# Kernel tuning notes

Hardware: AMD Instinct MI355X
Metric: run time of the kernel (lower is better)

Reference implementation:

```python
import jax, jax.numpy as jnp
import numpy as np

# Model constants (match init_kwargs and fla GatedLinearAttention defaults used in source)
L = 4            # num_layers
D = 1024         # d_model
H = 4            # n_heads
DK = 128         # head key dim  = 0.5*D / H
DV = 256         # head value dim = 1.0*D / H
KD = H * DK      # total key dim = 512
VD = H * DV      # total value dim = 1024
V = 32000        # vocab
B, T = 1, 2048
LR = 16          # gate_low_rank_dim
GLN = 16.0       # gate_logit_normalizer
EPS = 1e-5
SCALE = DK ** -0.5


def setup_inputs() -> dict:
    key = jax.random.key(0)
    ks = jax.random.split(key, 12)
    s = 0.02
    return {
        "input_ids": jax.random.randint(ks[0], (B, T), 0, V),
        "emb": jax.random.normal(ks[1], (V, D), jnp.float32) * s,
        "Wq": jax.random.normal(ks[2], (L, D, KD), jnp.float32) * s,
        "Wk": jax.random.normal(ks[3], (L, D, KD), jnp.float32) * s,
        "Wv": jax.random.normal(ks[4], (L, D, VD), jnp.float32) * s,
        "Wg": jax.random.normal(ks[5], (L, D, VD), jnp.float32) * s,
        "Wgk1": jax.random.normal(ks[6], (L, D, LR), jnp.float32) * s,
        "Wgk2": jax.random.normal(ks[7], (L, LR, KD), jnp.float32) * s,
        "bgk": jnp.zeros((L, KD), jnp.float32),
        "gnw": jnp.ones((L, DV), jnp.float32),
        "Wo": jax.random.normal(ks[8], (L, VD, D), jnp.float32) * s,
        "ln_w": jnp.ones((D,), jnp.float32),
        "ln_b": jnp.zeros((D,), jnp.float32),
        "Wlm": jax.random.normal(ks[9], (D, V), jnp.float32) * s,
        "blm": jnp.zeros((V,), jnp.float32),
    }


def _gla_layer(x, wq, wk, wv, wg, wg1, wg2, bg, nw, wo):
    # x: [B, T, D]
    b, t, _ = x.shape
    q = (x @ wq).reshape(b, t, H, DK) * SCALE
    k = (x @ wk).reshape(b, t, H, DK)
    v = (x @ wv).reshape(b, t, H, DV)
    g = (x @ wg).reshape(b, t, H, DV)
    # low-rank forget gate, log-space, normalized
    gk = (jax.nn.log_sigmoid((x @ wg1) @ wg2 + bg) / GLN).reshape(b, t, H, DK)

    # time-major for scan: [T, B, H, *]
    qt, kt, vt, gkt = (jnp.moveaxis(a, 1, 0) for a in (q, k, v, gk))

    def step(S, inp):
        q_t, k_t, v_t, gk_t = inp  # [B,H,DK], [B,H,DK], [B,H,DV], [B,H,DK]
        S = S * jnp.exp(gk_t)[..., None] + k_t[..., None] * v_t[..., None, :]
        o_t = jnp.einsum('bhk,bhkv->bhv', q_t, S)
        return S, o_t

    S0 = jnp.zeros((b, H, DK, DV), x.dtype)
    _, o = jax.lax.scan(step, S0, (qt, kt, vt, gkt))
    o = jnp.moveaxis(o, 0, 1)  # [B, T, H, DV]
    # fused RMSNorm + swish output gate
    o = o * jax.lax.rsqrt(jnp.mean(o * o, axis=-1, keepdims=True) + EPS) * nw
    o = o * (g * jax.nn.sigmoid(g))
    return o.reshape(b, t, VD) @ wo


def reference(input_ids, emb, Wq, Wk, Wv, Wg, Wgk1, Wgk2, bgk, gnw, Wo, ln_w, ln_b, Wlm, blm):
    h = emb[input_ids]  # [B, T, D]
    for i in range(L):
        h = _gla_layer(h, Wq[i], Wk[i], Wv[i], Wg[i], Wgk1[i], Wgk2[i], bgk[i], gnw[i], Wo[i])
    mu = jnp.mean(h, axis=-1, keepdims=True)
    var = jnp.mean((h - mu) ** 2, axis=-1, keepdims=True)
    h = (h - mu) * jax.lax.rsqrt(var + EPS) * ln_w + ln_b
    return h @ Wlm + blm
```

## Files before the change

kernel.cpp:

```cpp
#include <hip/hip_runtime.h>
#include <hip/hip_bf16.h>
#include <math.h>

#define NL 4
#define TT 2048
#define DD 1024
#define KDIM 512
#define VDIM 1024
#define QSTR 3072
#define NH 4
#define DKH 128
#define DVH 256
#define CH 64
#define NCH 32
#define VOCAB 32000
#define SCALE_Q 0.08838834764831845f

typedef short bf16x8 __attribute__((ext_vector_type(8)));
typedef float f32x4 __attribute__((ext_vector_type(4)));

__device__ __forceinline__ void gload_lds16(const void* g, void* l) {
    __builtin_amdgcn_global_load_lds((const __attribute__((address_space(1))) void*)g,
                                     (__attribute__((address_space(3))) void*)l, 16, 0, 0);
}

__device__ __forceinline__ void store_bf16x4(__hip_bfloat16* p, float a, float b, float c, float d) {
    union { __hip_bfloat16 h[4]; ushort4 v; } r;
    r.h[0] = __float2bfloat16(a); r.h[1] = __float2bfloat16(b);
    r.h[2] = __float2bfloat16(c); r.h[3] = __float2bfloat16(d);
    *(ushort4*)p = r.v;
}

__global__ __launch_bounds__(256) void embed_kernel(const int* __restrict__ ids,
                                                    const float* __restrict__ emb,
                                                    float* __restrict__ h,
                                                    __hip_bfloat16* __restrict__ hb) {
    int idx = blockIdx.x * 256 + threadIdx.x;
    int t = idx >> 8, c4 = idx & 255;
    float4 v = *(const float4*)(emb + (size_t)ids[t] * DD + c4 * 4);
    *(float4*)(h + (size_t)t * DD + c4 * 4) = v;
    store_bf16x4(hb + (size_t)t * DD + c4 * 4, v.x, v.y, v.z, v.w);
}

__global__ __launch_bounds__(256) void tconv_kernel(const float* __restrict__ in,
                                                    __hip_bfloat16* __restrict__ out,
                                                    int K, int N) {
    __shared__ float tle[64][65];
    const int n0 = blockIdx.x * 64, k0 = blockIdx.y * 64;
    const int tid = threadIdx.x;
    const int ty = tid >> 4, tx = tid & 15;
#pragma unroll
    for (int u = 0; u < 4; u++) {
        int r = ty + u * 16;
        float4 v = *(const float4*)(in + (size_t)(k0 + r) * N + n0 + tx * 4);
        tle[r][tx * 4 + 0] = v.x; tle[r][tx * 4 + 1] = v.y;
        tle[r][tx * 4 + 2] = v.z; tle[r][tx * 4 + 3] = v.w;
    }
    __syncthreads();
#pragma unroll
    for (int u = 0; u < 4; u++) {
        int nn = u * 16 + ty;
        store_bf16x4(out + (size_t)(n0 + nn) * K + k0 + tx * 4,
                     tle[tx * 4 + 0][nn], tle[tx * 4 + 1][nn],
                     tle[tx * 4 + 2][nn], tle[tx * 4 + 3][nn]);
    }
}

__global__ __launch_bounds__(256) void tconv_layer_kernel(const float* __restrict__ wq,
                                                          const float* __restrict__ wk,
                                                          const float* __restrict__ wv,
                                                          const float* __restrict__ wg,
                                                          const float* __restrict__ wo,
                                                          __hip_bfloat16* __restrict__ Wt,
                                                          __hip_bfloat16* __restrict__ WoT) {
    __shared__ float tle[64][65];
    int b = blockIdx.x;
    const float* src; __hip_bfloat16* dst; int N, local;
    if (b < 128)      { src = wq; dst = Wt;                         N = 512;  local = b; }
    else if (b < 256) { src = wk; dst = Wt + (size_t)512 * 1024;    N = 512;  local = b - 128; }
    else if (b < 512) { src = wv; dst = Wt + (size_t)1024 * 1024;   N = 1024; local = b - 256; }
    else if (b < 768) { src = wg; dst = Wt + (size_t)2048 * 1024;   N = 1024; local = b - 512; }
    else              { src = wo; dst = WoT;                        N = 1024; local = b - 768; }
    int nbx = N >> 6;
    int n0 = (local % nbx) * 64, k0 = (local / nbx) * 64;
    const int tid = threadIdx.x;
    const int ty = tid >> 4, tx = tid & 15;
#pragma unroll
    for (int u = 0; u < 4; u++) {
        int r = ty + u * 16;
        float4 v = *(const float4*)(src + (size_t)(k0 + r) * N + n0 + tx * 4);
        tle[r][tx * 4 + 0] = v.x; tle[r][tx * 4 + 1] = v.y;
        tle[r][tx * 4 + 2] = v.z; tle[r][tx * 4 + 3] = v.w;
    }
    __syncthreads();
#pragma unroll
    for (int u = 0; u < 4; u++) {
        int nn = u * 16 + ty;
        store_bf16x4(dst + (size_t)(n0 + nn) * 1024 + k0 + tx * 4,
                     tle[tx * 4 + 0][nn], tle[tx * 4 + 1][nn],
                     tle[tx * 4 + 2][nn], tle[tx * 4 + 3][nn]);
    }
}

template<int NF>
__global__ __launch_bounds__(256) void gemm_bf16_db(const __hip_bfloat16* __restrict__ A,
                                                    const __hip_bfloat16* __restrict__ Bt,
                                                    const float* __restrict__ bias,
                                                    float* __restrict__ C,
                                                    __hip_bfloat16* __restrict__ Cb,
                                                    int M, int N, int K) {
    __shared__ short a_lds[2][128 * 32];
    __shared__ short b_lds[2][NF * 32 * 32];
    const int tid = threadIdx.x;
    const int wv = tid >> 6, lane = tid & 63;
    const int wr = wv >> 1, wc = wv & 1;
    const int nbx = gridDim.x;
    int wg = blockIdx.y * nbx + blockIdx.x;
    int cpx = (nbx * gridDim.y) >> 3;
    int swz = (wg & 7) * cpx + (wg >> 3);
    const int m0 = (swz % nbx) * 128, n0 = (swz / nbx) * (NF * 32);
    const int lr = lane & 15, lk = (lane >> 4) * 8;

    f32x4 acc[4][NF];
#pragma unroll
    for (int m = 0; m < 4; m++)
#pragma unroll
        for (int n = 0; n < NF; n++) acc[m][n] = (f32x4)(0.f);

    auto STAGE = [&](int buf, int k0) {
#pragma unroll
        for (int u = 0; u < 2; u++) {
            int s = wv * 128 + u * 64 + lane;
            int r = s >> 2, kc = (s & 3) * 8;
            gload_lds16(A + (size_t)(m0 + r) * K + k0 + kc,
                        &a_lds[buf][(wv * 128 + u * 64) * 8]);
        }
        if constexpr (NF == 4) {
#pragma unroll
            for (int u = 0; u < 2; u++) {
                int s = wv * 128 + u * 64 + lane;
                int r = s >> 2, kc = (s & 3) * 8;
                gload_lds16(Bt + (size_t)(n0 + r) * K + k0 + kc,
                            &b_lds[buf][(wv * 128 + u * 64) * 8]);
            }
        } else {
            int s = wv * 64 + lane;
            int r = s >> 2, kc = (s & 3) * 8;
            gload_lds16(Bt + (size_t)(n0 + r) * K + k0 + kc,
                        &b_lds[buf][(wv * 64) * 8]);
        }
    };
    auto COMPUTE = [&](int buf) {
        bf16x8 af[4], bfr[NF];
#pragma unroll
        for (int m = 0; m < 4; m++)
            af[m] = *(const bf16x8*)&a_lds[buf][(wr * 64 + m * 16 + lr) * 32 + lk];
#pragma unroll
        for (int n = 0; n < NF; n++)
            bfr[n] = *(const bf16x8*)&b_lds[buf][(wc * (NF * 16) + n * 16 + lr) * 32 + lk];
#pragma unroll
        for (int m = 0; m < 4; m++)
#pragma unroll
            for (int n = 0; n < NF; n++)
                acc[m][n] = __builtin_amdgcn_mfma_f32_16x16x32_bf16(af[m], bfr[n], acc[m][n], 0, 0, 0);
    };

    STAGE(0, 0);
    __syncthreads();
    int cur = 0;
    for (int k0 = 32; k0 < K; k0 += 32) {
        STAGE(cur ^ 1, k0);
        COMPUTE(cur);
        __syncthreads();
        cur ^= 1;
    }
    COMPUTE(cur);

    const int rbase = (lane >> 4) * 4;
#pragma unroll
    for (int n = 0; n < NF; n++) {
        int col = n0 + wc * (NF * 16) + n * 16 + lr;
        float bv = bias ? bias[col] : 0.f;
#pragma unroll
        for (int m = 0; m < 4; m++) {
            int row = m0 + wr * 64 + m * 16 + rbase;
#pragma unroll
            for (int r = 0; r < 4; r++) {
                float val = acc[m][n][r] + bv;
                C[(size_t)(row + r) * N + col] = val;
                if (Cb) Cb[(size_t)(row + r) * N + col] = __float2bfloat16(val);
            }
        }
    }
}

__global__ __launch_bounds__(512, 1) void gemm256_lm(const __hip_bfloat16* __restrict__ A,
                                                     const __hip_bfloat16* __restrict__ Bt,
                                                     const float* __restrict__ bias,
                                                     float* __restrict__ C,
                                                     int M, int N, int K) {
    extern __shared__ __align__(16) char smem[];
    char* aB = smem;
    char* bB = smem + 2 * 16384;
    const int tid = threadIdx.x;
    const int wv = tid >> 6, lane = tid & 63;
    const int wr = wv >> 2, wc = wv & 3;
    const int lr = lane & 15, lk2 = ((lane >> 4) * 8) * 2;

    const int nbx = gridDim.x;
    int wg = blockIdx.y * nbx + blockIdx.x;
    int cpx = (nbx * gridDim.y) >> 3;
    int swz = (wg & 7) * cpx + (wg >> 3);
    const int m0 = (swz % nbx) * 256;
    const int n0 = (swz / nbx) * 256;

    auto STAGE = [&](const __hip_bfloat16* src, int row0, char* dst, int kt) {
#pragma unroll
        for (int i = 0; i < 2; i++) {
            int o = (wv * 2 + i) * 1024;
            int ob = o + lane * 16;
            int lg = ob ^ (((ob >> 7) & 7) << 4);
            int row = lg >> 6;
            int ce = (lg & 63) >> 1;
            gload_lds16(src + (size_t)(row0 + row) * K + kt * 32 + ce, dst + o);
        }
    };
    auto FRAG = [&](const char* buf, int row) -> bf16x8 {
        int lg = ((row >> 1) << 7) + ((row & 1) << 6) + lk2;
        return *(const bf16x8*)(buf + (lg ^ (((row >> 1) & 7) << 4)));
    };

    f32x4 acc[8][4];
#pragma unroll
    for (int m = 0; m < 8; m++)
#pragma unroll
        for (int n = 0; n < 4; n++) acc[m][n] = (f32x4)(0.f);

    const int NT = K / 32;
    STAGE(A,  m0, aB + 0 * 16384, 0);
    STAGE(Bt, n0, bB + 0 * 16384, 0);
    STAGE(Bt, n0, bB + 1 * 16384, 1);
    asm volatile("s_waitcnt vmcnt(2)" ::: "memory");
    __builtin_amdgcn_s_barrier();

    for (int t = 0; t < NT; t++) {
        const char* ab = aB + (t & 1) * 16384;
        const char* bb = bB + (t % 3) * 16384;
        int ta = t + 1 < NT ? t + 1 : NT - 1;
        STAGE(A, m0, aB + ((t + 1) & 1) * 16384, ta);
        int tb = t + 2 < NT ? t + 2 : NT - 1;
        STAGE(Bt, n0, bB + ((t + 2) % 3) * 16384, tb);

        bf16x8 bfr[4], af[8];
#pragma unroll
        for (int n = 0; n < 4; n++) bfr[n] = FRAG(bb, wc * 64 + n * 16 + lr);
#pragma unroll
        for (int m = 0; m < 8; m++) af[m] = FRAG(ab, wr * 128 + m * 16 + lr);
        __builtin_amdgcn_s_setprio(1);
#pragma unroll
        for (int m = 0; m < 8; m++)
#pragma unroll
            for (int n = 0; n < 4; n++)
                acc[m][n] = __builtin_amdgcn_mfma_f32_16x16x32_bf16(af[m], bfr[n], acc[m][n], 0, 0, 0);
        __builtin_amdgcn_s_setprio(0);
        asm volatile("s_waitcnt vmcnt(2)" ::: "memory");
        __builtin_amdgcn_s_barrier();
    }

    const int r4 = (lane >> 4) * 4;
#pragma unroll
    for (int n = 0; n < 4; n++) {
        int col = n0 + wc * 64 + n * 16 + lr;
        float bv = bias ? bias[col] : 0.f;
#pragma unroll
        for (int m = 0; m < 8; m++) {
            int row = m0 + wr * 128 + m * 16 + r4;
#pragma unroll
            for (int r = 0; r < 4; r++)
                C[(size_t)(row + r) * N + col] = acc[m][n][r] + bv;
        }
    }
}

__global__ __launch_bounds__(256) void lowrank1_kernel(const float* __restrict__ h,
                                                       const float* __restrict__ W1,
                                                       float* __restrict__ xg) {
    int t = blockIdx.x;
    int tid = threadIdx.x;
    int j = tid & 15, ks = tid >> 4;
    const float* hr = h + (size_t)t * DD + ks * 64;
    const float* w = W1 + (size_t)(ks * 64) * 16 + j;
    float acc = 0.f;
#pragma unroll 8
    for (int kk = 0; kk < 64; kk++) acc = fmaf(hr[kk], w[kk * 16], acc);
    __shared__ float red[16][17];
    red[ks][j] = acc;
    __syncthreads();
    if (tid < 16) {
        float s = 0.f;
#pragma unroll
        for (int r = 0; r < 16; r++) s += red[r][tid];
        xg[t * 16 + tid] = s;
    }
}

__global__ __launch_bounds__(256) void lowrank2_kernel(const float* __restrict__ xg,
                                                       const float* __restrict__ W2,
                                                       const float* __restrict__ bg,
                                                       float* __restrict__ gk) {
    int idx = blockIdx.x * 256 + threadIdx.x;
    int t = idx >> 9, n = idx & 511;
    const float* xr = xg + t * 16;
    float s = bg[n];
#pragma unroll
    for (int r = 0; r < 16; r++) s = fmaf(xr[r], W2[r * KDIM + n], s);
    float ls = fminf(s, 0.f) - log1pf(expf(-fabsf(s)));
    gk[idx] = ls * (1.f / 16.f);
}

__global__ __launch_bounds__(256) void gatescan_kernel(const float* __restrict__ qkvg,
                                                       const float* __restrict__ gk,
                                                       float* __restrict__ Gl,
                                                       __hip_bfloat16* __restrict__ qhB,
                                                       __hip_bfloat16* __restrict__ khB,
                                                       __hip_bfloat16* __restrict__ ktT) {
    int idx = blockIdx.x * 256 + threadIdx.x;
    int c = idx >> 9, col = idx & 511;
    float G = 0.f;
    float kh[64];
#pragma unroll
    for (int t = 0; t < 64; t++) {
        G += gk[(size_t)(c * 64 + t) * KDIM + col];
        const float* qp = qkvg + (size_t)(c * 64 + t) * QSTR + col;
        float qv = qp[0], kv = qp[512];
        qhB[(size_t)(c * 64 + t) * KDIM + col] = __float2bfloat16(qv * expf(G) * SCALE_Q);
        float khv = kv * expf(-G);
        khB[(size_t)(c * 64 + t) * KDIM + col] = __float2bfloat16(khv);
        kh[t] = khv;
    }
    Gl[idx] = G;
    float eGl = expf(G);
    int hh = col >> 7, dk = col & 127;
    __hip_bfloat16* kp = ktT + ((size_t)(c * NH + hh) * DKH + dk) * CH;
#pragma unroll
    for (int t = 0; t < 64; t++) kp[t] = __float2bfloat16(kh[t] * eGl);
}

__global__ __launch_bounds__(256) void vtrans_kernel(const float* __restrict__ qkvg,
                                                     __hip_bfloat16* __restrict__ vT) {
    __shared__ float tle[64][65];
    int bid = blockIdx.x;
    int dvq = bid & 3, hh = (bid >> 2) & 3, c = bid >> 4;
    int tid = threadIdx.x, ty = tid >> 4, tx = tid & 15;
#pragma unroll
    for (int u = 0; u < 4; u++) {
        int r = u * 16 + ty;
        float4 v = *(const float4*)(qkvg + (size_t)(c * 64 + r) * QSTR + 1024 + hh * DVH + dvq * 64 + tx * 4);
        tle[r][tx * 4 + 0] = v.x; tle[r][tx * 4 + 1] = v.y;
        tle[r][tx * 4 + 2] = v.z; tle[r][tx * 4 + 3] = v.w;
    }
    __syncthreads();
    __hip_bfloat16* dst = vT + ((size_t)(c * NH + hh) * DVH + dvq * 64) * CH;
#pragma unroll
    for (int u = 0; u < 4; u++) {
        int dv = u * 16 + ty;
        store_bf16x4(dst + (size_t)dv * CH + tx * 4,
                     tle[tx * 4 + 0][dv], tle[tx * 4 + 1][dv],
                     tle[tx * 4 + 2][dv], tle[tx * 4 + 3][dv]);
    }
}

__global__ __launch_bounds__(256) void chunkU_mfma(const __hip_bfloat16* __restrict__ vT,
                                                   const __hip_bfloat16* __restrict__ ktT,
                                                   __hip_bfloat16* __restrict__ U) {
    const int ch = blockIdx.x;
    const __hip_bfloat16* Ap = vT + (size_t)ch * DVH * CH;
    const __hip_bfloat16* Bp = ktT + (size_t)ch * DKH * CH;
    __hip_bfloat16* Cp = U + (size_t)ch * DVH * DKH;
    const int tid = threadIdx.x, wv = tid >> 6, lane = tid & 63;
    const int wr = wv >> 1, wc = wv & 1;
    const int lr = lane & 15, lk = (lane >> 4) * 8;
    f32x4 acc[8][4];
#pragma unroll
    for (int m = 0; m < 8; m++)
#pragma unroll
        for (int n = 0; n < 4; n++) acc[m][n] = (f32x4)(0.f);
#pragma unroll
    for (int ks = 0; ks < 2; ks++) {
        bf16x8 a[8], b[4];
#pragma unroll
        for (int m = 0; m < 8; m++)
            a[m] = *(const bf16x8*)(Ap + (size_t)(wr * 128 + m * 16 + lr) * CH + ks * 32 + lk);
#pragma unroll
        for (int n = 0; n < 4; n++)
            b[n] = *(const bf16x8*)(Bp + (size_t)(wc * 64 + n * 16 + lr) * CH + ks * 32 + lk);
#pragma unroll
        for (int m = 0; m < 8; m++)
#pragma unroll
            for (int n = 0; n < 4; n++)
                acc[m][n] = __builtin_amdgcn_mfma_f32_16x16x32_bf16(a[m], b[n], acc[m][n], 0, 0, 0);
    }
    const int r4 = (lane >> 4) * 4;
#pragma unroll
    for (int m = 0; m < 8; m++)
#pragma unroll
        for (int n = 0; n < 4; n++)
#pragma unroll
            for (int r = 0; r < 4; r++)
                Cp[(size_t)(wr * 128 + m * 16 + r4 + r) * DKH + wc * 64 + n * 16 + lr] =
                    __float2bfloat16(acc[m][n][r]);
}

__global__ __launch_bounds__(256) void scan_states_kernel(__hip_bfloat16* __restrict__ U,
                                                          const float* __restrict__ Gl) {
    int idx = blockIdx.x * 256 + threadIdx.x;
    int hh = idx >> 15, dv = (idx >> 7) & 255, dk = idx & 127;
    int col = hh * DKH + dk;
    float s = 0.f;
    for (int c = 0; c < NCH; c++) {
        __hip_bfloat16* p = U + ((size_t)(c * NH + hh) * DVH + dv) * DKH + dk;
        float u = __bfloat162float(*p);
        *p = __float2bfloat16(s);
        s = s * expf(Gl[c * KDIM + col]) + u;
    }
}

__global__ __launch_bounds__(256) void attn_rms_mfma(const __hip_bfloat16* __restrict__ qhB,
                                                     const __hip_bfloat16* __restrict__ khB,
                                                     const __hip_bfloat16* __restrict__ vT,
                                                     const __hip_bfloat16* __restrict__ Ub,
                                                     const float* __restrict__ qkvg,
                                                     const float* __restrict__ nw,
                                                     __hip_bfloat16* __restrict__ obb) {
    __shared__ __hip_bfloat16 P[32 * 72];
    __shared__ float sums[32][2];
    const int bid = blockIdx.x;
    const int rh = bid & 1, hh = (bid >> 1) & 3, c = bid >> 3;
    const int t0 = c * CH;
    const int tid = threadIdx.x, wv = tid >> 6, lane = tid & 63;
    const int half = wv >> 1, rg = wv & 1;
    const int lr = lane & 15, lk = (lane >> 4) * 8;
    const int r4 = (lane >> 4) * 4;
    const int rr = rh * 32 + rg * 16;

    bf16x8 qf[4];
#pragma unroll
    for (int ks = 0; ks < 4; ks++)
        qf[ks] = *(const bf16x8*)(qhB + (size_t)(t0 + rr + lr) * KDIM + hh * DKH + ks * 32 + lk);

    if (half == 0) {
        f32x4 s[4];
#pragma unroll
        for (int n = 0; n < 4; n++) s[n] = (f32x4)(0.f);
#pragma unroll
        for (int n = 0; n < 4; n++)
#pragma unroll
            for (int ks = 0; ks < 4; ks++) {
                bf16x8 kf = *(const bf16x8*)(khB + (size_t)(t0 + n * 16 + lr) * KDIM + hh * DKH + ks * 32 + lk);
                s[n] = __builtin_amdgcn_mfma_f32_16x16x32_bf16(qf[ks], kf, s[n], 0, 0, 0);
            }
#pragma unroll
        for (int n = 0; n < 4; n++)
#pragma unroll
            for (int r = 0; r < 4; r++) {
                int i = rr + r4 + r, j = n * 16 + lr;
                float val = (j <= i) ? s[n][r] : 0.f;
                P[(rg * 16 + r4 + r) * 72 + j] = __float2bfloat16(val);
            }
    }
    __syncthreads();

    const __hip_bfloat16* vTp = vT + ((size_t)(c * NH + hh) * DVH + half * 128) * CH;
    const __hip_bfloat16* Ubp = Ub + ((size_t)(c * NH + hh) * DVH + half * 128) * DKH;
    bf16x8 pf[2];
#pragma unroll
    for (int ks = 0; ks < 2; ks++)
        pf[ks] = *(const bf16x8*)&P[(rg * 16 + lr) * 72 + ks * 32 + lk];

    f32x4 o[8];
#pragma unroll
    for (int n = 0; n < 8; n++) o[n] = (f32x4)(0.f);
#pragma unroll
    for (int n = 0; n < 8; n++) {
#pragma unroll
        for (int ks = 0; ks < 2; ks++) {
            bf16x8 vf = *(const bf16x8*)(vTp + (size_t)(n * 16 + lr) * CH + ks * 32 + lk);
            o[n] = __builtin_amdgcn_mfma_f32_16x16x32_bf16(pf[ks], vf, o[n], 0, 0, 0);
        }
#pragma unroll
        for (int ks = 0; ks < 4; ks++) {
            bf16x8 uf = *(const bf16x8*)(Ubp + (size_t)(n * 16 + lr) * DKH + ks * 32 + lk);
            o[n] = __builtin_amdgcn_mfma_f32_16x16x32_bf16(qf[ks], uf, o[n], 0, 0, 0);
        }
    }

    float part[4];
#pragma unroll
    for (int r = 0; r < 4; r++) {
        float p = 0.f;
#pragma unroll
        for (int n = 0; n < 8; n++) p = fmaf(o[n][r], o[n][r], p);
        part[r] = p;
    }
#pragma unroll
    for (int off = 1; off < 16; off <<= 1)
#pragma unroll
        for (int r = 0; r < 4; r++) part[r] += __shfl_xor(part[r], off);
    if (lr == 0)
#pragma unroll
        for (int r = 0; r < 4; r++) sums[rg * 16 + r4 + r][half] = part[r];
    __syncthreads();

#pragma unroll
    for (int r = 0; r < 4; r++) {
        int lrow = rg * 16 + r4 + r;
        int t = t0 + rh * 32 + lrow;
        float tot = sums[lrow][0] + sums[lrow][1];
        float rinv = rsqrtf(tot * (1.f / 256.f) + 1e-5f);
#pragma unroll
        for (int n = 0; n < 8; n++) {
            int col = half * 128 + n * 16 + lr;
            float gv = qkvg[(size_t)t * QSTR + 2048 + hh * DVH + col];
            float val = o[n][r] * rinv * nw[col] * (gv / (1.f + expf(-gv)));
            obb[(size_t)t * VDIM + hh * DVH + col] = __float2bfloat16(val);
        }
    }
}

__global__ __launch_bounds__(256) void ln_kernel(const float* __restrict__ h,
                                                 const float* __restrict__ w,
                                                 const float* __restrict__ b,
                                                 __hip_bfloat16* __restrict__ out16) {
    int t = blockIdx.x;
    int tid = threadIdx.x;
    float4 x = *(const float4*)(h + (size_t)t * DD + tid * 4);
    float s = x.x + x.y + x.z + x.w;
    float ss = x.x * x.x + x.y * x.y + x.z * x.z + x.w * x.w;
#pragma unroll
    for (int off = 32; off > 0; off >>= 1) {
        s += __shfl_xor(s, off);
        ss += __shfl_xor(ss, off);
    }
    __shared__ float rs[4], rss[4];
    int wv = tid >> 6;
    if ((tid & 63) == 0) { rs[wv] = s; rss[wv] = ss; }
    __syncthreads();
    s = rs[0] + rs[1] + rs[2] + rs[3];
    ss = rss[0] + rss[1] + rss[2] + rss[3];
    float mu = s * (1.f / 1024.f);
    float var = ss * (1.f / 1024.f) - mu * mu;
    float r = rsqrtf(var + 1e-5f);
    float4 wv4 = *(const float4*)(w + tid * 4);
    float4 bv4 = *(const float4*)(b + tid * 4);
    store_bf16x4(out16 + (size_t)t * DD + tid * 4,
                 (x.x - mu) * r * wv4.x + bv4.x,
                 (x.y - mu) * r * wv4.y + bv4.y,
                 (x.z - mu) * r * wv4.z + bv4.z,
                 (x.w - mu) * r * wv4.w + bv4.w);
}

extern "C" void kernel_launch(void* const* d_in, const int* in_sizes, int n_in,
                              void* d_out, int out_size, void* d_ws, size_t ws_size,
                              hipStream_t stream) {
    const int*   ids  = (const int*)d_in[0];
    const float* emb  = (const float*)d_in[1];
    const float* Wq   = (const float*)d_in[2];
    const float* Wk   = (const float*)d_in[3];
    const float* Wv   = (const float*)d_in[4];
    const float* Wg   = (const float*)d_in[5];
    const float* Wgk1 = (const float*)d_in[6];
    const float* Wgk2 = (const float*)d_in[7];
    const float* bgk  = (const float*)d_in[8];
    const float* gnw  = (const float*)d_in[9];
    const float* Wo   = (const float*)d_in[10];
    const float* lnw  = (const float*)d_in[11];
    const float* lnb  = (const float*)d_in[12];
    const float* Wlm  = (const float*)d_in[13];
    const float* blm  = (const float*)d_in[14];
    float* out = (float*)d_out;

    float* ws = (float*)d_ws;
    float* h    = ws; ws += (size_t)TT * DD;
    float* qkvg = ws; ws += (size_t)TT * QSTR;
    float* gk   = ws; ws += (size_t)TT * KDIM;
    float* xg   = ws; ws += (size_t)TT * 16;
    float* Gl   = ws; ws += (size_t)NCH * KDIM;
    __hip_bfloat16* hb    = (__hip_bfloat16*)ws; ws += (size_t)TT * DD / 2;
    __hip_bfloat16* obb   = (__hip_bfloat16*)ws; ws += (size_t)TT * DD / 2;
    __hip_bfloat16* lnb16 = (__hip_bfloat16*)ws; ws += (size_t)TT * DD / 2;
    __hip_bfloat16* qhB   = (__hip_bfloat16*)ws; ws += (size_t)TT * KDIM / 2;
    __hip_bfloat16* khB   = (__hip_bfloat16*)ws; ws += (size_t)TT * KDIM / 2;
    __hip_bfloat16* ktT   = (__hip_bfloat16*)ws; ws += (size_t)NCH * NH * DKH * CH / 2;
    __hip_bfloat16* vT    = (__hip_bfloat16*)ws; ws += (size_t)NCH * NH * DVH * CH / 2;
    __hip_bfloat16* Ub    = (__hip_bfloat16*)ws; ws += (size_t)NCH * NH * DVH * DKH / 2;
    __hip_bfloat16* Wt    = (__hip_bfloat16*)ws; ws += (size_t)QSTR * DD / 2;
    __hip_bfloat16* WoT   = (__hip_bfloat16*)ws; ws += (size_t)VDIM * DD / 2;
    __hip_bfloat16* WlmT  = (__hip_bfloat16*)ws; ws += (size_t)VOCAB * DD / 2;

    hipFuncSetAttribute((const void*)gemm256_lm,
                        hipFuncAttributeMaxDynamicSharedMemorySize, 81920);

    embed_kernel<<<TT, 256, 0, stream>>>(ids, emb, h, hb);
    tconv_kernel<<<dim3(VOCAB / 64, DD / 64), 256, 0, stream>>>(Wlm, WlmT, DD, VOCAB);

    for (int l = 0; l < NL; l++) {
        const float* w1 = Wgk1 + (size_t)l * DD * 16;
        const float* w2 = Wgk2 + (size_t)l * 16 * KDIM;
        const float* bg = bgk + (size_t)l * KDIM;
        const float* nw = gnw + (size_t)l * DVH;

        tconv_layer_kernel<<<1024, 256, 0, stream>>>(Wq + (size_t)l * DD * KDIM,
                                                     Wk + (size_t)l * DD * KDIM,
                                                     Wv + (size_t)l * DD * VDIM,
                                                     Wg + (size_t)l * DD * VDIM,
                                                     Wo + (size_t)l * VDIM * DD, Wt, WoT);
        gemm_bf16_db<4><<<dim3(TT / 128, QSTR / 128), 256, 0, stream>>>(hb, Wt, nullptr, qkvg, nullptr, TT, QSTR, DD);
        lowrank1_kernel<<<TT, 256, 0, stream>>>(h, w1, xg);
        lowrank2_kernel<<<TT * KDIM / 256, 256, 0, stream>>>(xg, w2, bg, gk);
        gatescan_kernel<<<NCH * KDIM / 256, 256, 0, stream>>>(qkvg, gk, Gl, qhB, khB, ktT);
        vtrans_kernel<<<NCH * NH * 4, 256, 0, stream>>>(qkvg, vT);
        chunkU_mfma<<<NCH * NH, 256, 0, stream>>>(vT, ktT, Ub);
        scan_states_kernel<<<NH * DVH * DKH / 256, 256, 0, stream>>>(Ub, Gl);
        attn_rms_mfma<<<NCH * NH * 2, 256, 0, stream>>>(qhB, khB, vT, Ub, qkvg, nw, obb);
        gemm_bf16_db<2><<<dim3(TT / 128, DD / 64), 256, 0, stream>>>(obb, WoT, nullptr, h, hb, TT, DD, VDIM);
    }

    ln_kernel<<<TT, 256, 0, stream>>>(h, lnw, lnb, lnb16);
    gemm256_lm<<<dim3(TT / 256, VOCAB / 256), 512, 81920, stream>>>(lnb16, WlmT, blm, out, TT, VOCAB, DD);
}
```

Baseline: 720.1 us.

## Restructure LM-head GEMM into 4-phase ping-pong pipeline with 64-wide K tiles

Rewrites the main loop of the 256x256 LM-head GEMM to use 64-wide K tiles with double-buffered A and B in 128KB of LDS. Each iteration is split into four phases, each computing a quarter of the M fragments while issuing one global-to-LDS stage, separated by barriers. The goal is to interleave loads with MFMA work more finely and reduce per-tile barrier and wait overhead. The cost is higher LDS use and more barriers per tile.

```diff
diff --git a/kernel.cpp b/kernel.cpp
--- a/kernel.cpp
+++ b/kernel.cpp
@@ -194,18 +194,73 @@
     }
 }
 
+__device__ __forceinline__ void lm_stage(const __hip_bfloat16* src, int row0,
+                                         char* dst, int kt32, int wv, int lane, int K) {
+#pragma unroll
+    for (int ii = 0; ii < 2; ii++) {
+        int o = (wv * 2 + ii) * 1024;
+        int ob = o + lane * 16;
+        int lg = ob ^ (((ob >> 7) & 7) << 4);
+        int row = lg >> 6;
+        int ce = (lg & 63) >> 1;
+        gload_lds16(src + (size_t)(row0 + row) * K + kt32 * 32 + ce, dst + o);
+    }
+}
+
+__device__ __forceinline__ bf16x8 lm_frag(const char* sub, int row, int lk2) {
+    int lg = ((row >> 1) << 7) + ((row & 1) << 6) + lk2;
+    return *(const bf16x8*)(sub + (lg ^ (((row >> 1) & 7) << 4)));
+}
+
+template<int PT, bool LOADB, int VM>
+__device__ __forceinline__ void lm_phase(const char* aT, const char* bT,
+                                         const __hip_bfloat16* ssrc, int srow0,
+                                         char* sdst, int skt32,
+                                         bf16x8 (&bfr)[4][2], f32x4 (&acc)[8][4],
+                                         int wr, int wc, int lr, int lk2,
+                                         int wv, int lane, int K) {
+    if constexpr (LOADB) {
+#pragma unroll
+        for (int n = 0; n < 4; n++)
+#pragma unroll
+            for (int ks = 0; ks < 2; ks++)
+                bfr[n][ks] = lm_frag(bT + ks * 16384, wc * 64 + n * 16 + lr, lk2);
+    }
+    bf16x8 af[2][2];
+#pragma unroll
+    for (int mm = 0; mm < 2; mm++)
+#pragma unroll
+        for (int ks = 0; ks < 2; ks++)
+            af[mm][ks] = lm_frag(aT + ks * 16384, wr * 128 + (2 * PT + mm) * 16 + lr, lk2);
+    lm_stage(ssrc, srow0, sdst, skt32, wv, lane, K);
+    asm volatile("s_barrier" ::: "memory");
+    __builtin_amdgcn_s_setprio(1);
+#pragma unroll
+    for (int mm = 0; mm < 2; mm++)
+#pragma unroll
+        for (int n = 0; n < 4; n++) {
+            acc[2 * PT + mm][n] = __builtin_amdgcn_mfma_f32_16x16x32_bf16(af[mm][0], bfr[n][0], acc[2 * PT + mm][n], 0, 0, 0);
+            acc[2 * PT + mm][n] = __builtin_amdgcn_mfma_f32_16x16x32_bf16(af[mm][1], bfr[n][1], acc[2 * PT + mm][n], 0, 0, 0);
+        }
+    __builtin_amdgcn_s_setprio(0);
+    if constexpr (VM == 4) asm volatile("s_waitcnt vmcnt(4)" ::: "memory");
+    asm volatile("s_barrier" ::: "memory");
+}
+
 __global__ __launch_bounds__(512, 1) void gemm256_lm(const __hip_bfloat16* __restrict__ A,
                                                      const __hip_bfloat16* __restrict__ Bt,
                                                      const float* __restrict__ bias,
                                                      float* __restrict__ C,
                                                      int M, int N, int K) {
     extern __shared__ __align__(16) char smem[];
-    char* aB = smem;
-    char* bB = smem + 2 * 16384;
+    char* sA0 = smem;
+    char* sA1 = smem + 32768;
+    char* sB0 = smem + 65536;
+    char* sB1 = smem + 98304;
     const int tid = threadIdx.x;
     const int wv = tid >> 6, lane = tid & 63;
     const int wr = wv >> 2, wc = wv & 3;
-    const int lr = lane & 15, lk2 = ((lane >> 4) * 8) * 2;
+    const int lr = lane & 15, lk2 = (lane >> 4) * 16;
 
     const int nbx = gridDim.x;
     int wg = blockIdx.y * nbx + blockIdx.x;
@@ -214,57 +269,37 @@
     const int m0 = (swz % nbx) * 256;
     const int n0 = (swz / nbx) * 256;
 
-    auto STAGE = [&](const __hip_bfloat16* src, int row0, char* dst, int kt) {
-#pragma unroll
-        for (int i = 0; i < 2; i++) {
-            int o = (wv * 2 + i) * 1024;
-            int ob = o + lane * 16;
-            int lg = ob ^ (((ob >> 7) & 7) << 4);
-            int row = lg >> 6;
-            int ce = (lg & 63) >> 1;
-            gload_lds16(src + (size_t)(row0 + row) * K + kt * 32 + ce, dst + o);
-        }
-    };
-    auto FRAG = [&](const char* buf, int row) -> bf16x8 {
-        int lg = ((row >> 1) << 7) + ((row & 1) << 6) + lk2;
-        return *(const bf16x8*)(buf + (lg ^ (((row >> 1) & 7) << 4)));
-    };
-
     f32x4 acc[8][4];
 #pragma unroll
     for (int m = 0; m < 8; m++)
 #pragma unroll
         for (int n = 0; n < 4; n++) acc[m][n] = (f32x4)(0.f);
 
-    const int NT = K / 32;
-    STAGE(A,  m0, aB + 0 * 16384, 0);
-    STAGE(Bt, n0, bB + 0 * 16384, 0);
-    STAGE(Bt, n0, bB + 1 * 16384, 1);
-    asm volatile("s_waitcnt vmcnt(2)" ::: "memory");
-    __builtin_amdgcn_s_barrier();
-
-    for (int t = 0; t < NT; t++) {
-        const char* ab = aB + (t & 1) * 16384;
-        const char* bb = bB + (t % 3) * 16384;
-        int ta = t + 1 < NT ? t + 1 : NT - 1;
-        STAGE(A, m0, aB + ((t + 1) & 1) * 16384, ta);
-        int tb = t + 2 < NT ? t + 2 : NT - 1;
-        STAGE(Bt, n0, bB + ((t + 2) % 3) * 16384, tb);
-
-        bf16x8 bfr[4], af[8];
-#pragma unroll
-        for (int n = 0; n < 4; n++) bfr[n] = FRAG(bb, wc * 64 + n * 16 + lr);
-#pragma unroll
-        for (int m = 0; m < 8; m++) af[m] = FRAG(ab, wr * 128 + m * 16 + lr);
-        __builtin_amdgcn_s_setprio(1);
-#pragma unroll
-        for (int m = 0; m < 8; m++)
-#pragma unroll
-            for (int n = 0; n < 4; n++)
-                acc[m][n] = __builtin_amdgcn_mfma_f32_16x16x32_bf16(af[m], bfr[n], acc[m][n], 0, 0, 0);
-        __builtin_amdgcn_s_setprio(0);
-        asm volatile("s_waitcnt vmcnt(2)" ::: "memory");
-        __builtin_amdgcn_s_barrier();
+    const int NTI = K / 64;
+    const int NI  = NTI / 2;
+
+    lm_stage(A,  m0, sA0 + 0,     0, wv, lane, K);
+    lm_stage(A,  m0, sA0 + 16384, 1, wv, lane, K);
+    lm_stage(Bt, n0, sB0 + 0,     0, wv, lane, K);
+    lm_stage(Bt, n0, sB0 + 16384, 1, wv, lane, K);
+    lm_stage(Bt, n0, sB1 + 0,     2, wv, lane, K);
+    lm_stage(Bt, n0, sB1 + 16384, 3, wv, lane, K);
+    asm volatile("s_waitcnt vmcnt(0)" ::: "memory");
+    asm volatile("s_barrier" ::: "memory");
+
+    for (int i = 0; i < NI; i++) {
+        int tOdd = 2 * i + 1;
+        int tE   = 2 * i + 2 < NTI ? 2 * i + 2 : NTI - 1;
+        int tB3  = 2 * i + 3 < NTI ? 2 * i + 3 : NTI - 1;
+        bf16x8 bfr[4][2];
+        lm_phase<0, true , 0>(sA0, sB0, A,  m0, sA1 + 0,     2 * tOdd + 0, bfr, acc, wr, wc, lr, lk2, wv, lane, K);
+        lm_phase<1, false, 0>(sA0, sB0, A,  m0, sA1 + 16384, 2 * tOdd + 1, bfr, acc, wr, wc, lr, lk2, wv, lane, K);
+        lm_phase<2, false, 0>(sA0, sB0, Bt, n0, sB0 + 0,     2 * tE   + 0, bfr, acc, wr, wc, lr, lk2, wv, lane, K);
+        lm_phase<3, false, 4>(sA0, sB0, Bt, n0, sB0 + 16384, 2 * tE   + 1, bfr, acc, wr, wc, lr, lk2, wv, lane, K);
+        lm_phase<0, true , 0>(sA1, sB1, A,  m0, sA0 + 0,     2 * tE   + 0, bfr, acc, wr, wc, lr, lk2, wv, lane, K);
+        lm_phase<1, false, 0>(sA1, sB1, A,  m0, sA0 + 16384, 2 * tE   + 1, bfr, acc, wr, wc, lr, lk2, wv, lane, K);
+        lm_phase<2, false, 0>(sA1, sB1, Bt, n0, sB1 + 0,     2 * tB3  + 0, bfr, acc, wr, wc, lr, lk2, wv, lane, K);
+        lm_phase<3, false, 4>(sA1, sB1, Bt, n0, sB1 + 16384, 2 * tB3  + 1, bfr, acc, wr, wc, lr, lk2, wv, lane, K);
     }
 
     const int r4 = (lane >> 4) * 4;
@@ -598,7 +633,7 @@
     __hip_bfloat16* WlmT  = (__hip_bfloat16*)ws; ws += (size_t)VOCAB * DD / 2;
 
     hipFuncSetAttribute((const void*)gemm256_lm,
-                        hipFuncAttributeMaxDynamicSharedMemorySize, 81920);
+                        hipFuncAttributeMaxDynamicSharedMemorySize, 131072);
 
     embed_kernel<<<TT, 256, 0, stream>>>(ids, emb, h, hb);
     tconv_kernel<<<dim3(VOCAB / 64, DD / 64), 256, 0, stream>>>(Wlm, WlmT, DD, VOCAB);
@@ -626,5 +661,5 @@
     }
 
     ln_kernel<<<TT, 256, 0, stream>>>(h, lnw, lnb, lnb16);
-    gemm256_lm<<<dim3(TT / 256, VOCAB / 256), 512, 81920, stream>>>(lnb16, WlmT, blm, out, TT, VOCAB, DD);
-}
+    gemm256_lm<<<dim3(TT / 256, VOCAB / 256), 512, 131072, stream>>>(lnb16, WlmT, blm, out, TT, VOCAB, DD);
+}
```

Measured after the change: 706.1 us. Within noise of the previous version (-1.9%).
